# Performance work log

Measured on AMD Instinct MI355X. Metric: run time of the kernel, lower is better.

Reference implementation:

```python
import jax, jax.numpy as jnp
import numpy as np

DIM = 1024
HEADS = 16
DIM_HEAD = 64
INNER = HEADS * DIM_HEAD  # 1024
SCALE = DIM_HEAD ** -0.5


def setup_inputs() -> dict:
    key = jax.random.key(0)
    k1, k2, k3, k4, k5 = jax.random.split(key, 5)
    x = jax.random.normal(k1, (4, 2048, DIM), dtype=jnp.float32)
    w_qkv = jax.random.normal(k2, (DIM, 3 * INNER), dtype=jnp.float32) * (DIM ** -0.5)
    b_qkv = jax.random.normal(k3, (3 * INNER,), dtype=jnp.float32) * 0.02
    w_out = jax.random.normal(k4, (INNER, DIM), dtype=jnp.float32) * (INNER ** -0.5)
    b_out = jax.random.normal(k5, (DIM,), dtype=jnp.float32) * 0.02
    return {"x": x, "w_qkv": w_qkv, "b_qkv": b_qkv, "w_out": w_out, "b_out": b_out}


def reference(x, w_qkv, b_qkv, w_out, b_out):
    b, n, _ = x.shape
    qkv = x @ w_qkv + b_qkv  # [b, n, 3*inner]
    q, k, v = jnp.split(qkv, 3, axis=-1)
    # b n (h d) -> b h n d
    def split_heads(t):
        return t.reshape(b, n, HEADS, DIM_HEAD).transpose(0, 2, 1, 3)
    q, k, v = map(split_heads, (q, k, v))
    scores = jnp.einsum('bhnd,bhmd->bhnm', q, k) * SCALE  # [b, h, n, n]
    att = jax.nn.softmax(scores, axis=-1)
    out = jnp.einsum('bhnm,bhmd->bhnd', att, v)  # [b, h, n, d]
    out = out.transpose(0, 2, 1, 3).reshape(b, n, INNER)  # b h n d -> b n (h d)
    return out @ w_out + b_out
```

## Files before the change

kernel.cpp:

```cpp
#include <hip/hip_runtime.h>
#include <stdint.h>

typedef float f32x4 __attribute__((ext_vector_type(4)));
typedef short s16x8 __attribute__((ext_vector_type(8)));
typedef unsigned short u16;
typedef unsigned short u16x4v __attribute__((ext_vector_type(4)));
typedef unsigned int u32x2 __attribute__((ext_vector_type(2)));

__device__ __forceinline__ u16 f2bf(float x) {
  union { float f; uint32_t u; } c; c.f = x;
  uint32_t u = c.u + 0x7fffu + ((c.u >> 16) & 1u);
  return (u16)(u >> 16);
}

__device__ __forceinline__ void async16(void* lds, const void* g) {
  __builtin_amdgcn_global_load_lds(
      (const __attribute__((address_space(1))) uint32_t*)(uintptr_t)g,
      (__attribute__((address_space(3))) uint32_t*)(uintptr_t)lds,
      16, 0, 0);
}

__device__ __forceinline__ uint32_t pack_bf2(float f0, float f1) {
  uint32_t u0 = __builtin_bit_cast(uint32_t, f0) + 0x8000u;
  uint32_t u1 = __builtin_bit_cast(uint32_t, f1) + 0x8000u;
  return __builtin_amdgcn_perm(u1, u0, 0x07060302u);
}

#define CSCALE 0.18033688011112042f

__global__ __launch_bounds__(256) void cvt_bf16_kernel(
    const float* __restrict__ in, u16* __restrict__ out) {
  size_t i = ((size_t)blockIdx.x * 256 + threadIdx.x) * 4;
  f32x4 v = *(const f32x4*)(in + i);
  u16x4v o;
#pragma unroll
  for (int j = 0; j < 4; ++j) o[j] = f2bf(v[j]);
  *(u16x4v*)(out + i) = o;
}

__global__ __launch_bounds__(256) void transpose_cvt(
    const float* __restrict__ in, u16* __restrict__ out, int R, int C) {
  __shared__ float t[32][33];
  int tx = threadIdx.x & 31, ty = threadIdx.x >> 5;
  int r0 = blockIdx.y * 32, c0 = blockIdx.x * 32;
#pragma unroll
  for (int i = 0; i < 4; ++i)
    t[ty + i * 8][tx] = in[(size_t)(r0 + ty + i * 8) * C + c0 + tx];
  __syncthreads();
#pragma unroll
  for (int i = 0; i < 4; ++i)
    out[(size_t)(c0 + ty + i * 8) * R + r0 + tx] = f2bf(t[tx][ty + i * 8]);
}

template <int MODE>
__global__ __launch_bounds__(256, 3) void gemm_bt(
    const u16* __restrict__ A, const u16* __restrict__ Bt,
    const float* __restrict__ bias,
    u16* __restrict__ qd, u16* __restrict__ kd, u16* __restrict__ vtd,
    float* __restrict__ outd) {
  __shared__ u16 lA[128 * 32];
  __shared__ u16 lB[128 * 32];
  const int tid = threadIdx.x;
  const int lane = tid & 63;
  const int quad = lane >> 4;
  const int l15 = lane & 15;
  const int wv = tid >> 6;
  const int wm = wv >> 1, wn = wv & 1;
  const int m0 = blockIdx.y * 128;
  const int n0 = blockIdx.x * 128;

  f32x4 acc[4][4] = {};

  const char* Ab = (const char*)A + (size_t)m0 * 2048;
  const char* Bb = (const char*)Bt + (size_t)n0 * 2048;
  const int o0 = tid * 16;
  const int o1 = 4096 + tid * 16;
  const char* a0 = Ab + (size_t)(o0 >> 6) * 2048 + (o0 & 63);
  const char* a1 = Ab + (size_t)(o1 >> 6) * 2048 + (o1 & 63);
  const char* b0 = Bb + (size_t)(o0 >> 6) * 2048 + (o0 & 63);
  const char* b1 = Bb + (size_t)(o1 >> 6) * 2048 + (o1 & 63);

  for (int kt = 0; kt < 2048; kt += 64) {
    __syncthreads();
    async16((char*)lA + o0, a0 + kt);
    async16((char*)lA + o1, a1 + kt);
    async16((char*)lB + o0, b0 + kt);
    async16((char*)lB + o1, b1 + kt);
    __syncthreads();
    s16x8 af[4], bf[4];
#pragma unroll
    for (int g = 0; g < 4; ++g) {
      af[g] = *(const s16x8*)((const char*)lA + (wm * 64 + g * 16 + l15) * 64 + quad * 16);
      bf[g] = *(const s16x8*)((const char*)lB + (wn * 64 + g * 16 + l15) * 64 + quad * 16);
    }
#pragma unroll
    for (int i = 0; i < 4; ++i)
#pragma unroll
      for (int j = 0; j < 4; ++j)
        acc[i][j] = __builtin_amdgcn_mfma_f32_16x16x32_bf16(af[i], bf[j], acc[i][j], 0, 0, 0);
  }

  float bj[4];
#pragma unroll
  for (int j = 0; j < 4; ++j) bj[j] = bias[n0 + wn * 64 + j * 16 + l15];

  if (MODE == 0) {
#pragma unroll
    for (int j = 0; j < 4; ++j) {
      int col = n0 + wn * 64 + j * 16 + l15;
      int which = col >> 10;
      int rem = col & 1023;
      int h = rem >> 6, d = rem & 63;
#pragma unroll
      for (int i = 0; i < 4; ++i) {
#pragma unroll
        for (int r = 0; r < 4; ++r) {
          int row = m0 + wm * 64 + i * 16 + quad * 4 + r;
          int b = row >> 11, s = row & 2047;
          float t = acc[i][j][r] + bj[j];
          if (which == 0) t *= CSCALE;
          u16 v = f2bf(t);
          size_t bh = (size_t)(b * 16 + h);
          if (which == 0)      qd[(bh * 2048 + s) * 64 + d] = v;
          else if (which == 1) kd[(bh * 2048 + s) * 64 + d] = v;
          else                 vtd[(bh * 64 + d) * 2048 + s] = v;
        }
      }
    }
  } else {
#pragma unroll
    for (int i = 0; i < 4; ++i)
#pragma unroll
      for (int r = 0; r < 4; ++r) {
        int row = m0 + wm * 64 + i * 16 + quad * 4 + r;
#pragma unroll
        for (int j = 0; j < 4; ++j) {
          int col = n0 + wn * 64 + j * 16 + l15;
          outd[(size_t)row * 1024 + col] = acc[i][j][r] + bj[j];
        }
      }
  }
}

__global__ __launch_bounds__(256, 2) void attn_fused(
    const u16* __restrict__ Q, const u16* __restrict__ Kd,
    const u16* __restrict__ Vt, u16* __restrict__ Od) {
  __shared__ u16 lK[2][4096];
  __shared__ u16 lV[2][4096];
  const int tid = threadIdx.x;
  const int lane = tid & 63;
  const int wv = tid >> 6;
  const int quad = lane >> 4;
  const int l15 = lane & 15;
  const int bh = blockIdx.x & 63;
  const int qt = blockIdx.x >> 6;
  const int q0 = qt * 256 + wv * 64;

  const u16* qb = Q + ((size_t)bh * 2048 + q0) * 64;
  const char* kbB = (const char*)(Kd + (size_t)bh * 2048 * 64);
  const char* vbB = (const char*)(Vt + (size_t)bh * 64 * 2048);

  const int r0 = tid >> 3, s0 = tid & 7;
  const int r1 = r0 + 32;
  const int kOff0 = r0 * 128 + ((s0 ^ (r0 & 7)) * 16);
  const int kOff1 = r1 * 128 + ((s0 ^ (r1 & 7)) * 16);
  const int vOff0 = r0 * 4096 + ((s0 ^ (r0 & 7)) * 16);
  const int vOff1 = r1 * 4096 + ((s0 ^ (r1 & 7)) * 16);

  auto stage = [&](int kbase, int buf) {
    const char* ks = kbB + (size_t)kbase * 128;
    const char* vs = vbB + (size_t)kbase * 2;
    async16((char*)lK[buf] + tid * 16, ks + kOff0);
    async16((char*)lK[buf] + 4096 + tid * 16, ks + kOff1);
    async16((char*)lV[buf] + tid * 16, vs + vOff0);
    async16((char*)lV[buf] + 4096 + tid * 16, vs + vOff1);
  };

  s16x8 qfr[4][2];
#pragma unroll
  for (int qf = 0; qf < 4; ++qf)
#pragma unroll
    for (int kd2 = 0; kd2 < 2; ++kd2)
      qfr[qf][kd2] = *(const s16x8*)(qb + (qf * 16 + l15) * 64 + kd2 * 32 + quad * 8);

  s16x8 ones;
#pragma unroll
  for (int j = 0; j < 8; ++j) ones[j] = (short)0x3F80;

  f32x4 oacc[4][4] = {};
  f32x4 lacc[4] = {};

  const int sw = (l15 & 7);

  auto compute = [&](int buf) {
    const char* bK = (const char*)lK[buf];
    const char* bV = (const char*)lV[buf];

    uint32_t pd[4][4][2];
#pragma unroll
    for (int mf = 0; mf < 4; ++mf) {
      const char* kr = bK + (mf * 16 + l15) * 128;
      s16x8 kf0 = *(const s16x8*)(kr + ((quad ^ sw) * 16));
      s16x8 kf1 = *(const s16x8*)(kr + (((4 + quad) ^ sw) * 16));
      f32x4 st[4];
#pragma unroll
      for (int qf = 0; qf < 4; ++qf) {
        f32x4 a = {};
        a = __builtin_amdgcn_mfma_f32_16x16x32_bf16(kf0, qfr[qf][0], a, 0, 0, 0);
        a = __builtin_amdgcn_mfma_f32_16x16x32_bf16(kf1, qfr[qf][1], a, 0, 0, 0);
        st[qf] = a;
      }
#pragma unroll
      for (int qf = 0; qf < 4; ++qf) {
        float p0 = __builtin_amdgcn_exp2f(st[qf][0]);
        float p1 = __builtin_amdgcn_exp2f(st[qf][1]);
        float p2 = __builtin_amdgcn_exp2f(st[qf][2]);
        float p3 = __builtin_amdgcn_exp2f(st[qf][3]);
        pd[mf][qf][0] = pack_bf2(p0, p1);
        pd[mf][qf][1] = pack_bf2(p2, p3);
      }
    }

    s16x8 vf[4][2];
#pragma unroll
    for (int df = 0; df < 4; ++df) {
      const char* vr = bV + (df * 16 + l15) * 128;
#pragma unroll
      for (int kh = 0; kh < 2; ++kh)
        vf[df][kh] = *(const s16x8*)(vr + (((kh * 4 + quad) ^ sw) * 16));
    }

#pragma unroll
    for (int kh = 0; kh < 2; ++kh)
#pragma unroll
      for (int qf = 0; qf < 4; ++qf)
#pragma unroll
        for (int pi = 0; pi < 2; ++pi) {
          uint32_t x = pd[2 * kh][qf][pi];
          uint32_t y = pd[2 * kh + 1][qf][pi];
          asm("s_nop 1\n\t"
              "v_permlane32_swap_b32 %0, %1\n\t"
              "s_nop 0\n\t"
              "v_permlane16_swap_b32 %0, %1"
              : "+v"(x), "+v"(y));
          pd[2 * kh][qf][pi] = x;
          pd[2 * kh + 1][qf][pi] = y;
        }

#pragma unroll
    for (int kh = 0; kh < 2; ++kh)
#pragma unroll
      for (int qf = 0; qf < 4; ++qf) {
        union { s16x8 h; uint32_t u[4]; } bfr;
        bfr.u[0] = pd[2 * kh][qf][0];
        bfr.u[1] = pd[2 * kh][qf][1];
        bfr.u[2] = pd[2 * kh + 1][qf][0];
        bfr.u[3] = pd[2 * kh + 1][qf][1];
#pragma unroll
        for (int df = 0; df < 4; ++df)
          oacc[df][qf] = __builtin_amdgcn_mfma_f32_16x16x32_bf16(vf[df][kh], bfr.h, oacc[df][qf], 0, 0, 0);
        lacc[qf] = __builtin_amdgcn_mfma_f32_16x16x32_bf16(ones, bfr.h, lacc[qf], 0, 0, 0);
      }
  };

  stage(0, 0);
  __syncthreads();
#pragma unroll 1
  for (int t = 0; t < 32; t += 2) {
    if (t + 1 < 32) stage((t + 1) * 64, 1);
    compute(0);
    __syncthreads();
    if (t + 2 < 32) stage((t + 2) * 64, 0);
    compute(1);
    __syncthreads();
  }

  const int b = bh >> 4, h = bh & 15;
  float inv[4];
#pragma unroll
  for (int qf = 0; qf < 4; ++qf) inv[qf] = 1.0f / lacc[qf][0];
#pragma unroll
  for (int qf = 0; qf < 4; ++qf) {
    u16* rowp = Od + ((size_t)b * 2048 + q0 + qf * 16 + l15) * 1024 + h * 64;
#pragma unroll
    for (int df = 0; df < 4; ++df) {
      u32x2 w;
      w.x = pack_bf2(oacc[df][qf][0] * inv[qf], oacc[df][qf][1] * inv[qf]);
      w.y = pack_bf2(oacc[df][qf][2] * inv[qf], oacc[df][qf][3] * inv[qf]);
      *(u32x2*)(rowp + df * 16 + quad * 4) = w;
    }
  }
}

extern "C" void kernel_launch(void* const* d_in, const int* in_sizes, int n_in,
                              void* d_out, int out_size, void* d_ws, size_t ws_size,
                              hipStream_t stream) {
  const float* x = (const float*)d_in[0];
  const float* w_qkv = (const float*)d_in[1];
  const float* b_qkv = (const float*)d_in[2];
  const float* w_out = (const float*)d_in[3];
  const float* b_out = (const float*)d_in[4];
  float* out = (float*)d_out;
  char* ws = (char*)d_ws;

  u16* xb    = (u16*)(ws + 0);
  u16* wqkvT = (u16*)(ws + 16777216);
  u16* woutT = (u16*)(ws + 23068672);
  u16* qw    = (u16*)(ws + 25165824);
  u16* kw    = (u16*)(ws + 41943040);
  u16* vtw   = (u16*)(ws + 58720256);
  u16* attO  = (u16*)(ws + 75497472);

  cvt_bf16_kernel<<<8192, 256, 0, stream>>>(x, xb);
  transpose_cvt<<<dim3(96, 32), 256, 0, stream>>>(w_qkv, wqkvT, 1024, 3072);
  transpose_cvt<<<dim3(32, 32), 256, 0, stream>>>(w_out, woutT, 1024, 1024);
  gemm_bt<0><<<dim3(24, 64), 256, 0, stream>>>(xb, wqkvT, b_qkv, qw, kw, vtw, nullptr);
  attn_fused<<<512, 256, 0, stream>>>(qw, kw, vtw, attO);
  gemm_bt<1><<<dim3(8, 64), 256, 0, stream>>>(attO, woutT, b_out, nullptr, nullptr, nullptr, out);
}
```

Before: 289.2 us.

## Rewrite bf16 GEMM with 256x128 tiles, triple-buffered swizzled LDS pipeline

```diff
diff --git a/kernel.cpp b/kernel.cpp
--- a/kernel.cpp
+++ b/kernel.cpp
@@ -53,52 +53,111 @@
 }
 
 template <int MODE>
-__global__ __launch_bounds__(256, 3) void gemm_bt(
+__global__ __launch_bounds__(512, 2) void gemm_bt(
     const u16* __restrict__ A, const u16* __restrict__ Bt,
     const float* __restrict__ bias,
     u16* __restrict__ qd, u16* __restrict__ kd, u16* __restrict__ vtd,
     float* __restrict__ outd) {
-  __shared__ u16 lA[128 * 32];
-  __shared__ u16 lB[128 * 32];
+  __shared__ u16 lA[3][256 * 64];
+  __shared__ u16 lB[3][128 * 64];
   const int tid = threadIdx.x;
   const int lane = tid & 63;
   const int quad = lane >> 4;
   const int l15 = lane & 15;
   const int wv = tid >> 6;
-  const int wm = wv >> 1, wn = wv & 1;
-  const int m0 = blockIdx.y * 128;
-  const int n0 = blockIdx.x * 128;
+  const int wm = wv >> 1;
+  const int wn = wv & 1;
+
+  constexpr int GX = (MODE == 0) ? 24 : 8;
+  constexpr int CPX = (GX * 32) / 8;
+  int bid = blockIdx.y * GX + blockIdx.x;
+  bid = (bid & 7) * CPX + (bid >> 3);
+  const int m0 = (bid / GX) * 256;
+  const int n0 = (bid % GX) * 128;
+
+  const char* aSrc[4];
+  int aOff[4];
+#pragma unroll
+  for (int c2 = 0; c2 < 4; ++c2) {
+    int c = c2 * 512 + tid, r = c >> 3, s = c & 7, g = s ^ (r & 7);
+    aSrc[c2] = (const char*)A + (size_t)(m0 + r) * 2048 + g * 16;
+    aOff[c2] = c * 16;
+  }
+  const char* bSrc[2];
+  int bOff[2];
+#pragma unroll
+  for (int c2 = 0; c2 < 2; ++c2) {
+    int c = c2 * 512 + tid, r = c >> 3, s = c & 7, g = s ^ (r & 7);
+    bSrc[c2] = (const char*)Bt + (size_t)(n0 + r) * 2048 + g * 16;
+    bOff[c2] = c * 16;
+  }
 
   f32x4 acc[4][4] = {};
-
-  const char* Ab = (const char*)A + (size_t)m0 * 2048;
-  const char* Bb = (const char*)Bt + (size_t)n0 * 2048;
-  const int o0 = tid * 16;
-  const int o1 = 4096 + tid * 16;
-  const char* a0 = Ab + (size_t)(o0 >> 6) * 2048 + (o0 & 63);
-  const char* a1 = Ab + (size_t)(o1 >> 6) * 2048 + (o1 & 63);
-  const char* b0 = Bb + (size_t)(o0 >> 6) * 2048 + (o0 & 63);
-  const char* b1 = Bb + (size_t)(o1 >> 6) * 2048 + (o1 & 63);
-
-  for (int kt = 0; kt < 2048; kt += 64) {
-    __syncthreads();
-    async16((char*)lA + o0, a0 + kt);
-    async16((char*)lA + o1, a1 + kt);
-    async16((char*)lB + o0, b0 + kt);
-    async16((char*)lB + o1, b1 + kt);
-    __syncthreads();
-    s16x8 af[4], bf[4];
-#pragma unroll
-    for (int g = 0; g < 4; ++g) {
-      af[g] = *(const s16x8*)((const char*)lA + (wm * 64 + g * 16 + l15) * 64 + quad * 16);
-      bf[g] = *(const s16x8*)((const char*)lB + (wn * 64 + g * 16 + l15) * 64 + quad * 16);
-    }
+  const int swA = l15 & 7;
+  const int arow = wm * 64 + l15;
+  const int brow = wn * 64 + l15;
+
+  auto phase = [&](const u16* bA, const u16* bB, int kh, int nb, int ko,
+                   bool stg, int sel) {
+    s16x8 af[4], bq[4];
 #pragma unroll
     for (int i = 0; i < 4; ++i)
+      af[i] = *(const s16x8*)((const char*)bA + (arow + i * 16) * 128 +
+                              (((kh << 2) | quad) ^ swA) * 16);
+#pragma unroll
+    for (int j = 0; j < 4; ++j)
+      bq[j] = *(const s16x8*)((const char*)bB + (brow + j * 16) * 128 +
+                              (((kh << 2) | quad) ^ swA) * 16);
+    if (stg) {
+      if (sel == 0) {
+        async16((char*)lA[nb] + aOff[0], aSrc[0] + ko);
+        async16((char*)lA[nb] + aOff[1], aSrc[1] + ko);
+        async16((char*)lB[nb] + bOff[0], bSrc[0] + ko);
+      } else {
+        async16((char*)lA[nb] + aOff[2], aSrc[2] + ko);
+        async16((char*)lA[nb] + aOff[3], aSrc[3] + ko);
+        async16((char*)lB[nb] + bOff[1], bSrc[1] + ko);
+      }
+    }
+    __builtin_amdgcn_s_setprio(1);
+#pragma unroll
+    for (int i = 0; i < 4; ++i)
 #pragma unroll
       for (int j = 0; j < 4; ++j)
-        acc[i][j] = __builtin_amdgcn_mfma_f32_16x16x32_bf16(af[i], bf[j], acc[i][j], 0, 0, 0);
-  }
+        acc[i][j] =
+            __builtin_amdgcn_mfma_f32_16x16x32_bf16(af[i], bq[j], acc[i][j], 0, 0, 0);
+    __builtin_amdgcn_s_setprio(0);
+  };
+
+#pragma unroll
+  for (int c2 = 0; c2 < 4; ++c2) async16((char*)lA[0] + aOff[c2], aSrc[c2]);
+#pragma unroll
+  for (int c2 = 0; c2 < 2; ++c2) async16((char*)lB[0] + bOff[c2], bSrc[c2]);
+#pragma unroll
+  for (int c2 = 0; c2 < 4; ++c2) async16((char*)lA[1] + aOff[c2], aSrc[c2] + 128);
+#pragma unroll
+  for (int c2 = 0; c2 < 2; ++c2) async16((char*)lB[1] + bOff[c2], bSrc[c2] + 128);
+  asm volatile("s_waitcnt vmcnt(6)" ::: "memory");
+  __builtin_amdgcn_s_barrier();
+
+  int bufc = 0;
+#pragma unroll 1
+  for (int t = 0; t < 14; ++t) {
+    const int nb = bufc >= 1 ? bufc - 1 : 2;
+    const int ko = (t + 2) * 128;
+    phase(lA[bufc], lB[bufc], 0, nb, ko, true, 0);
+    phase(lA[bufc], lB[bufc], 1, nb, ko, true, 1);
+    asm volatile("s_waitcnt vmcnt(6)" ::: "memory");
+    __builtin_amdgcn_s_barrier();
+    bufc = bufc < 2 ? bufc + 1 : 0;
+  }
+  phase(lA[bufc], lB[bufc], 0, 0, 0, false, 0);
+  phase(lA[bufc], lB[bufc], 1, 0, 0, false, 1);
+  asm volatile("s_waitcnt vmcnt(0)" ::: "memory");
+  __builtin_amdgcn_s_barrier();
+  bufc = bufc < 2 ? bufc + 1 : 0;
+  phase(lA[bufc], lB[bufc], 0, 0, 0, false, 0);
+  phase(lA[bufc], lB[bufc], 1, 0, 0, false, 1);
 
   float bj[4];
 #pragma unroll
@@ -314,7 +373,7 @@
   cvt_bf16_kernel<<<8192, 256, 0, stream>>>(x, xb);
   transpose_cvt<<<dim3(96, 32), 256, 0, stream>>>(w_qkv, wqkvT, 1024, 3072);
   transpose_cvt<<<dim3(32, 32), 256, 0, stream>>>(w_out, woutT, 1024, 1024);
-  gemm_bt<0><<<dim3(24, 64), 256, 0, stream>>>(xb, wqkvT, b_qkv, qw, kw, vtw, nullptr);
+  gemm_bt<0><<<dim3(24, 32), 512, 0, stream>>>(xb, wqkvT, b_qkv, qw, kw, vtw, nullptr);
   attn_fused<<<512, 256, 0, stream>>>(qw, kw, vtw, attO);
-  gemm_bt<1><<<dim3(8, 64), 256, 0, stream>>>(attO, woutT, b_out, nullptr, nullptr, nullptr, out);
-}
+  gemm_bt<1><<<dim3(8, 32), 512, 0, stream>>>(attO, woutT, b_out, nullptr, nullptr, nullptr, out);
+}
```

After: 276.1 us. 1.05x faster.

## Rewrite GEMM mainloop with 256x128 tiles, triple-buffered async loads, swizzled LDS

Applied to the files above, without the earlier changes.

```diff
diff --git a/kernel.cpp b/kernel.cpp
--- a/kernel.cpp
+++ b/kernel.cpp
@@ -53,52 +53,122 @@
 }
 
 template <int MODE>
-__global__ __launch_bounds__(256, 3) void gemm_bt(
+__global__ __launch_bounds__(512, 2) void gemm_bt(
     const u16* __restrict__ A, const u16* __restrict__ Bt,
     const float* __restrict__ bias,
     u16* __restrict__ qd, u16* __restrict__ kd, u16* __restrict__ vtd,
     float* __restrict__ outd) {
-  __shared__ u16 lA[128 * 32];
-  __shared__ u16 lB[128 * 32];
+  __shared__ u16 lA[3][256 * 64];
+  __shared__ u16 lB[3][128 * 64];
   const int tid = threadIdx.x;
   const int lane = tid & 63;
   const int quad = lane >> 4;
   const int l15 = lane & 15;
   const int wv = tid >> 6;
-  const int wm = wv >> 1, wn = wv & 1;
-  const int m0 = blockIdx.y * 128;
-  const int n0 = blockIdx.x * 128;
+  const int wm = wv >> 1;
+  const int wn = wv & 1;
+
+  constexpr int GX = (MODE == 0) ? 24 : 8;
+  constexpr int CPX = (GX * 32) / 8;
+  int bid = blockIdx.y * GX + blockIdx.x;
+  bid = (bid & 7) * CPX + (bid >> 3);
+  const int m0 = (bid / GX) * 256;
+  const int n0 = (bid % GX) * 128;
+
+  const char* aSrc0; const char* aSrc1; const char* aSrc2; const char* aSrc3;
+  const char* bSrc0; const char* bSrc1;
+  int aOff0, aOff1, aOff2, aOff3, bOff0, bOff1;
+  {
+    int c, r, s, g;
+    c = 0 * 512 + tid; r = c >> 3; s = c & 7; g = s ^ (r & 7);
+    aSrc0 = (const char*)A + (size_t)(m0 + r) * 2048 + g * 16; aOff0 = c * 16;
+    c = 1 * 512 + tid; r = c >> 3; s = c & 7; g = s ^ (r & 7);
+    aSrc1 = (const char*)A + (size_t)(m0 + r) * 2048 + g * 16; aOff1 = c * 16;
+    c = 2 * 512 + tid; r = c >> 3; s = c & 7; g = s ^ (r & 7);
+    aSrc2 = (const char*)A + (size_t)(m0 + r) * 2048 + g * 16; aOff2 = c * 16;
+    c = 3 * 512 + tid; r = c >> 3; s = c & 7; g = s ^ (r & 7);
+    aSrc3 = (const char*)A + (size_t)(m0 + r) * 2048 + g * 16; aOff3 = c * 16;
+    c = 0 * 512 + tid; r = c >> 3; s = c & 7; g = s ^ (r & 7);
+    bSrc0 = (const char*)Bt + (size_t)(n0 + r) * 2048 + g * 16; bOff0 = c * 16;
+    c = 1 * 512 + tid; r = c >> 3; s = c & 7; g = s ^ (r & 7);
+    bSrc1 = (const char*)Bt + (size_t)(n0 + r) * 2048 + g * 16; bOff1 = c * 16;
+  }
 
   f32x4 acc[4][4] = {};
-
-  const char* Ab = (const char*)A + (size_t)m0 * 2048;
-  const char* Bb = (const char*)Bt + (size_t)n0 * 2048;
-  const int o0 = tid * 16;
-  const int o1 = 4096 + tid * 16;
-  const char* a0 = Ab + (size_t)(o0 >> 6) * 2048 + (o0 & 63);
-  const char* a1 = Ab + (size_t)(o1 >> 6) * 2048 + (o1 & 63);
-  const char* b0 = Bb + (size_t)(o0 >> 6) * 2048 + (o0 & 63);
-  const char* b1 = Bb + (size_t)(o1 >> 6) * 2048 + (o1 & 63);
-
-  for (int kt = 0; kt < 2048; kt += 64) {
-    __syncthreads();
-    async16((char*)lA + o0, a0 + kt);
-    async16((char*)lA + o1, a1 + kt);
-    async16((char*)lB + o0, b0 + kt);
-    async16((char*)lB + o1, b1 + kt);
-    __syncthreads();
-    s16x8 af[4], bf[4];
-#pragma unroll
-    for (int g = 0; g < 4; ++g) {
-      af[g] = *(const s16x8*)((const char*)lA + (wm * 64 + g * 16 + l15) * 64 + quad * 16);
-      bf[g] = *(const s16x8*)((const char*)lB + (wn * 64 + g * 16 + l15) * 64 + quad * 16);
-    }
-#pragma unroll
-    for (int i = 0; i < 4; ++i)
-#pragma unroll
-      for (int j = 0; j < 4; ++j)
-        acc[i][j] = __builtin_amdgcn_mfma_f32_16x16x32_bf16(af[i], bf[j], acc[i][j], 0, 0, 0);
-  }
+  const int swA = l15 & 7;
+  const int aBase = (wm * 64 + l15) * 128;
+  const int bBase = (wn * 64 + l15) * 128;
+  const int swz0 = (quad ^ swA) * 16;
+  const int swz1 = ((4 | quad) ^ swA) * 16;
+  const char* lAc = (const char*)lA;
+  const char* lBc = (const char*)lB;
+  char* lAw = (char*)lA;
+  char* lBw = (char*)lB;
+
+#define GPH(CB, NB, KH, KO, STG)                                              \
+  {                                                                           \
+    s16x8 af[4], bq[4];                                                       \
+    const int so = (KH) ? swz1 : swz0;                                        \
+    _Pragma("unroll") for (int i = 0; i < 4; ++i)                             \
+      af[i] = *(const s16x8*)(lAc + (CB) * 32768 + aBase + i * 2048 + so);    \
+    _Pragma("unroll") for (int j = 0; j < 4; ++j)                             \
+      bq[j] = *(const s16x8*)(lBc + (CB) * 16384 + bBase + j * 2048 + so);    \
+    if (STG) {                                                                \
+      if ((KH) == 0) {                                                        \
+        async16(lAw + (NB) * 32768 + aOff0, aSrc0 + (KO));                    \
+        async16(lAw + (NB) * 32768 + aOff1, aSrc1 + (KO));                    \
+        async16(lBw + (NB) * 16384 + bOff0, bSrc0 + (KO));                    \
+      } else {                                                                \
+        async16(lAw + (NB) * 32768 + aOff2, aSrc2 + (KO));                    \
+        async16(lAw + (NB) * 32768 + aOff3, aSrc3 + (KO));                    \
+        async16(lBw + (NB) * 16384 + bOff1, bSrc1 + (KO));                    \
+      }                                                                       \
+    }                                                                         \
+    __builtin_amdgcn_sched_barrier(0);                                        \
+    __builtin_amdgcn_s_barrier();                                             \
+    asm volatile("s_waitcnt lgkmcnt(0)" ::: "memory");                        \
+    __builtin_amdgcn_sched_barrier(0);                                        \
+    __builtin_amdgcn_s_setprio(1);                                            \
+    _Pragma("unroll") for (int i = 0; i < 4; ++i)                             \
+      _Pragma("unroll") for (int j = 0; j < 4; ++j)                           \
+        acc[i][j] = __builtin_amdgcn_mfma_f32_16x16x32_bf16(af[i], bq[j],     \
+                                                            acc[i][j], 0, 0, 0); \
+    __builtin_amdgcn_s_setprio(0);                                            \
+    __builtin_amdgcn_sched_barrier(0);                                        \
+  }
+
+  async16(lAw + aOff0, aSrc0);
+  async16(lAw + aOff1, aSrc1);
+  async16(lAw + aOff2, aSrc2);
+  async16(lAw + aOff3, aSrc3);
+  async16(lBw + bOff0, bSrc0);
+  async16(lBw + bOff1, bSrc1);
+  async16(lAw + 32768 + aOff0, aSrc0 + 128);
+  async16(lAw + 32768 + aOff1, aSrc1 + 128);
+  async16(lAw + 32768 + aOff2, aSrc2 + 128);
+  async16(lAw + 32768 + aOff3, aSrc3 + 128);
+  async16(lBw + 16384 + bOff0, bSrc0 + 128);
+  async16(lBw + 16384 + bOff1, bSrc1 + 128);
+  asm volatile("s_waitcnt vmcnt(6)" ::: "memory");
+  __builtin_amdgcn_s_barrier();
+
+#define GTILE(T)                                                              \
+  GPH((T) % 3, ((T) + 2) % 3, 0, ((T) + 2) * 128, 1);                         \
+  GPH((T) % 3, ((T) + 2) % 3, 1, ((T) + 2) * 128, 1);                         \
+  asm volatile("s_waitcnt vmcnt(6)" ::: "memory");                            \
+  __builtin_amdgcn_s_barrier();
+
+  GTILE(0) GTILE(1) GTILE(2) GTILE(3) GTILE(4) GTILE(5) GTILE(6)
+  GTILE(7) GTILE(8) GTILE(9) GTILE(10) GTILE(11) GTILE(12) GTILE(13)
+#undef GTILE
+
+  GPH(2, 0, 0, 0, 0);
+  GPH(2, 0, 1, 0, 0);
+  asm volatile("s_waitcnt vmcnt(0)" ::: "memory");
+  __builtin_amdgcn_s_barrier();
+  GPH(0, 0, 0, 0, 0);
+  GPH(0, 0, 1, 0, 0);
+#undef GPH
 
   float bj[4];
 #pragma unroll
@@ -314,7 +384,7 @@
   cvt_bf16_kernel<<<8192, 256, 0, stream>>>(x, xb);
   transpose_cvt<<<dim3(96, 32), 256, 0, stream>>>(w_qkv, wqkvT, 1024, 3072);
   transpose_cvt<<<dim3(32, 32), 256, 0, stream>>>(w_out, woutT, 1024, 1024);
-  gemm_bt<0><<<dim3(24, 64), 256, 0, stream>>>(xb, wqkvT, b_qkv, qw, kw, vtw, nullptr);
+  gemm_bt<0><<<dim3(24, 32), 512, 0, stream>>>(xb, wqkvT, b_qkv, qw, kw, vtw, nullptr);
   attn_fused<<<512, 256, 0, stream>>>(qw, kw, vtw, attO);
-  gemm_bt<1><<<dim3(8, 64), 256, 0, stream>>>(attO, woutT, b_out, nullptr, nullptr, nullptr, out);
-}
+  gemm_bt<1><<<dim3(8, 32), 512, 0, stream>>>(attO, woutT, b_out, nullptr, nullptr, nullptr, out);
+}
```

Result: faster. 272.9 us (-5.7%).
